# Kernel tuning notes

Hardware: AMD Instinct MI355X
Metric: run time of the kernel (lower is better)

Reference implementation:

```python
import jax, jax.numpy as jnp
import numpy as np

DIM = 4096
N_HEAD = 32
N_KV_HEAD = 8
HEAD_DIM = DIM // N_HEAD  # 128
B, T = 2, 2048


def _rope_freqs(T, head_dim, theta=10000.0):
    inv = 1.0 / (theta ** (np.arange(0, head_dim, 2, dtype=np.float32) / head_dim))
    t = np.arange(T, dtype=np.float32)
    ang = np.outer(t, inv)  # [T, head_dim/2]
    return jnp.asarray(np.stack([np.cos(ang), np.sin(ang)], axis=-1))  # [T, hd/2, 2]


def setup_inputs() -> dict:
    key = jax.random.key(0)
    ks = jax.random.split(key, 5)
    s = 1.0 / np.sqrt(DIM)
    return {
        "x": jax.random.normal(ks[0], (B, T, DIM), dtype=jnp.float32),
        "freqs_cis": _rope_freqs(T, HEAD_DIM),
        "wq": jax.random.normal(ks[1], (DIM, N_HEAD * HEAD_DIM), dtype=jnp.float32) * s,
        "wk": jax.random.normal(ks[2], (DIM, N_KV_HEAD * HEAD_DIM), dtype=jnp.float32) * s,
        "wv": jax.random.normal(ks[3], (DIM, N_KV_HEAD * HEAD_DIM), dtype=jnp.float32) * s,
        "wo": jax.random.normal(ks[4], (DIM, DIM), dtype=jnp.float32) * s,
    }


def _apply_rotary(x, freqs_cis):
    # x: [B, T, H, head_dim]; freqs_cis: [T, head_dim/2, 2]
    xs = x.reshape(*x.shape[:-1], -1, 2)  # [B, T, H, hd/2, 2]
    fc = freqs_cis[None, :, None, :, :]   # [1, T, 1, hd/2, 2]
    real = xs[..., 0] * fc[..., 0] - xs[..., 1] * fc[..., 1]
    imag = xs[..., 1] * fc[..., 0] + xs[..., 0] * fc[..., 1]
    return jnp.stack([real, imag], axis=-1).reshape(x.shape)


def reference(x, freqs_cis, wq, wk, wv, wo):
    Bx, Tx, C = x.shape
    q = (x @ wq).reshape(Bx, Tx, N_HEAD, HEAD_DIM)
    k = (x @ wk).reshape(Bx, Tx, N_KV_HEAD, HEAD_DIM)
    v = (x @ wv).reshape(Bx, Tx, N_KV_HEAD, HEAD_DIM)
    q = _apply_rotary(q, freqs_cis)
    k = _apply_rotary(k, freqs_cis)
    # [B, H, T, hd]
    q = q.transpose(0, 2, 1, 3)
    k = k.transpose(0, 2, 1, 3)
    v = v.transpose(0, 2, 1, 3)
    # GQA: expand kv heads to match query heads
    rep = N_HEAD // N_KV_HEAD
    k = jnp.repeat(k, rep, axis=1)
    v = jnp.repeat(v, rep, axis=1)
    scale = 1.0 / np.sqrt(HEAD_DIM)
    scores = jnp.einsum("bhqd,bhkd->bhqk", q, k) * scale
    causal = jnp.tril(jnp.ones((Tx, Tx), dtype=bool))
    scores = jnp.where(causal[None, None], scores, jnp.float32(-1e30))
    attn = jax.nn.softmax(scores, axis=-1)
    y = jnp.einsum("bhqk,bhkd->bhqd", attn, v)
    y = y.transpose(0, 2, 1, 3).reshape(Bx, Tx, C)
    return y @ wo
```

## Files before the change

kernel.cpp:

```cpp
#include <hip/hip_runtime.h>

#define DIM  4096
#define NH   32
#define NKV  8
#define HD   128
#define BSZ  2
#define TSEQ 2048

typedef __bf16 bf16x8 __attribute__((ext_vector_type(8)));
typedef unsigned short ushort8v __attribute__((ext_vector_type(8)));
typedef float f32x4 __attribute__((ext_vector_type(4)));

typedef void GV __attribute__((address_space(1)));
typedef void LV __attribute__((address_space(3)));

__device__ __forceinline__ unsigned short f2bf(float f) {
  unsigned u = __builtin_bit_cast(unsigned, f);
  u += 0x7FFFu + ((u >> 16) & 1u);
  return (unsigned short)(u >> 16);
}
__device__ __forceinline__ float bf2f(unsigned short b) {
  unsigned u = ((unsigned)b) << 16;
  return __builtin_bit_cast(float, u);
}
__device__ __forceinline__ void gload16(const unsigned short* g, unsigned short* l) {
  __builtin_amdgcn_global_load_lds((GV*)g, (LV*)l, 16, 0, 0);
}
__device__ __forceinline__ f32x4 mfma16(bf16x8 a, bf16x8 b, f32x4 c) {
  return __builtin_amdgcn_mfma_f32_16x16x32_bf16(a, b, c, 0, 0, 0);
}
__device__ __forceinline__ bf16x8 lds8(const unsigned short* p) {
  return __builtin_bit_cast(bf16x8, *(const ushort8v*)p);
}

__global__ void detect_dtype(const unsigned int* __restrict__ fc, int* __restrict__ flag) {
  if (threadIdx.x == 0 && blockIdx.x == 0)
    *flag = (fc[0] == 0x3F800000u) ? 0 : 1;
}

__global__ void cast_x(const void* __restrict__ src, unsigned short* __restrict__ dst,
                       const int* __restrict__ flag) {
  long t = (long)blockIdx.x * 256 + threadIdx.x;
  if (*flag) {
    ((uint2*)dst)[t] = ((const uint2*)src)[t];
  } else {
    float4 f = ((const float4*)src)[t];
    ushort4 o;
    o.x = f2bf(f.x); o.y = f2bf(f.y); o.z = f2bf(f.z); o.w = f2bf(f.w);
    ((ushort4*)dst)[t] = o;
  }
}

__global__ __launch_bounds__(256) void transpose64(const void* __restrict__ src,
                                                   unsigned short* __restrict__ dst,
                                                   int R, int C, const int* __restrict__ flag) {
  __shared__ unsigned short tile[64][68];
  const int isbf = *flag;
  const int tid = threadIdx.x;
  const int c0g = blockIdx.x * 64, r0g = blockIdx.y * 64;
  const int cc = (tid & 15) * 4;
  if (isbf) {
    const unsigned short* s = (const unsigned short*)src;
#pragma unroll
    for (int it = 0; it < 4; ++it) {
      const int r = it * 16 + (tid >> 4);
      ushort4 v = *(const ushort4*)(s + (long)(r0g + r) * C + c0g + cc);
      *(ushort4*)&tile[r][cc] = v;
    }
  } else {
    const float* s = (const float*)src;
#pragma unroll
    for (int it = 0; it < 4; ++it) {
      const int r = it * 16 + (tid >> 4);
      float4 f = *(const float4*)(s + (long)(r0g + r) * C + c0g + cc);
      ushort4 v;
      v.x = f2bf(f.x); v.y = f2bf(f.y); v.z = f2bf(f.z); v.w = f2bf(f.w);
      *(ushort4*)&tile[r][cc] = v;
    }
  }
  __syncthreads();
#pragma unroll
  for (int it = 0; it < 2; ++it) {
    const int c = (tid >> 3) + it * 32;
    const int r0 = (tid & 7) * 8;
    ushort8v o;
#pragma unroll
    for (int u = 0; u < 8; ++u) o[u] = tile[r0 + u][c];
    *(ushort8v*)(dst + (long)(c0g + c) * R + r0g + r0) = o;
  }
}

__device__ __forceinline__ void gemm128_loop(const unsigned short* __restrict__ A,
                                             const unsigned short* __restrict__ Bt,
                                             unsigned short* As, unsigned short* Bs,
                                             long tileM, long tileN, f32x4 (&acc)[4][4]) {
  const int tid = (int)threadIdx.x;
  const int lane = tid & 63, wave = tid >> 6;
  const int wr = wave >> 1, wc = wave & 1;
  const int lm = lane & 15, quad = lane >> 4;
  const int sr = tid >> 3;
  const int schunk = ((tid & 7) ^ (sr & 7)) * 8;
  const unsigned short* Ag = A + (tileM + sr) * 4096L + schunk;
  const unsigned short* Bg = Bt + (tileN + sr) * 4096L + schunk;
  unsigned short* Al = As + sr * 64 + (tid & 7) * 8;
  unsigned short* Bl = Bs + sr * 64 + (tid & 7) * 8;

  auto stgA = [&](int slot, int half, int tt) {
    const unsigned short* g = Ag + (long)half * (64 * 4096L) + (long)tt * 64;
    unsigned short* l = Al + slot * 8192 + half * 4096;
    gload16(g, l);
    gload16(g + 32 * 4096L, l + 2048);
  };
  auto stgB = [&](int slot, int half, int tt) {
    const unsigned short* g = Bg + (long)half * (64 * 4096L) + (long)tt * 64;
    unsigned short* l = Bl + slot * 8192 + half * 4096;
    gload16(g, l);
    gload16(g + 32 * 4096L, l + 2048);
  };
  auto rdA = [&](int so, int f, int kk) {
    return lds8(&As[so + (wr * 64 + f * 16 + lm) * 64 + (((kk * 4 + quad) ^ (lm & 7)) * 8)]);
  };
  auto rdB = [&](int so, int f, int kk) {
    return lds8(&Bs[so + (wc * 64 + f * 16 + lm) * 64 + (((kk * 4 + quad) ^ (lm & 7)) * 8)]);
  };

  stgB(0, 0, 0); stgB(0, 1, 0); stgA(0, 0, 0); stgA(0, 1, 0);
  stgB(1, 0, 1); stgB(1, 1, 1); stgA(1, 0, 1);
  asm volatile("s_waitcnt vmcnt(6)" ::: "memory");
  __builtin_amdgcn_sched_barrier(0);
  __builtin_amdgcn_s_barrier();

#pragma unroll 2
  for (int t = 0; t < 64; ++t) {
    __builtin_amdgcn_sched_barrier(0);
    const int s = t & 1;
    const int so = s * 8192;
    bf16x8 a[4][2], b[4][2];
#pragma unroll
    for (int f = 0; f < 4; ++f) { a[f][0] = rdA(so, f, 0); a[f][1] = rdA(so, f, 1); }
#pragma unroll
    for (int f = 0; f < 4; ++f) { b[f][0] = rdB(so, f, 0); b[f][1] = rdB(so, f, 1); }
    if (t < 63) stgA(s ^ 1, 1, t + 1);
    asm volatile("s_waitcnt lgkmcnt(0)" ::: "memory");
    __builtin_amdgcn_sched_barrier(0);
    __builtin_amdgcn_s_setprio(1);
#pragma unroll
    for (int mf = 0; mf < 4; ++mf)
#pragma unroll
      for (int nf = 0; nf < 4; ++nf)
        acc[mf][nf] = mfma16(a[mf][0], b[nf][0], acc[mf][nf]);
    __builtin_amdgcn_s_setprio(0);
    __builtin_amdgcn_sched_barrier(0);
    __builtin_amdgcn_s_barrier();
    if (t < 62) { stgB(s, 0, t + 2); stgB(s, 1, t + 2); stgA(s, 0, t + 2); }
    __builtin_amdgcn_s_setprio(1);
#pragma unroll
    for (int mf = 0; mf < 4; ++mf)
#pragma unroll
      for (int nf = 0; nf < 4; ++nf)
        acc[mf][nf] = mfma16(a[mf][1], b[nf][1], acc[mf][nf]);
    __builtin_amdgcn_s_setprio(0);
    if (t < 62)       asm volatile("s_waitcnt vmcnt(6)" ::: "memory");
    else if (t == 62) asm volatile("s_waitcnt vmcnt(0)" ::: "memory");
    __builtin_amdgcn_sched_barrier(0);
    __builtin_amdgcn_s_barrier();
  }
}

__global__ __launch_bounds__(256, 2) void gemm_qkv8(const unsigned short* __restrict__ A,
                                                    const unsigned short* __restrict__ Bt,
                                                    const void* __restrict__ fcv,
                                                    const int* __restrict__ flag,
                                                    unsigned short* __restrict__ qo,
                                                    unsigned short* __restrict__ ko,
                                                    unsigned short* __restrict__ vo) {
  __shared__ __align__(16) unsigned short As[2 * 8192];
  __shared__ __align__(16) unsigned short Bs[2 * 8192];
  const int bid = (int)blockIdx.x;
  const int xcd = bid & 7, idx = bid >> 3;
  const int band = idx >> 6;
  const int rr = idx & 63;
  const long tileM = (long)((xcd & 3) * 8 + (rr & 7)) * 128;
  const long tileN = (long)((xcd >> 2) * 24 + band * 8 + (rr >> 3)) * 128;
  f32x4 acc[4][4] = {};
  gemm128_loop(A, Bt, As, Bs, tileM, tileN, acc);
  const int tid = (int)threadIdx.x;
  const int lane = tid & 63, wave = tid >> 6;
  const int wr = wave >> 1, wc = wave & 1;
  const int lm = lane & 15, quad = lane >> 4;
  const int isbf = *flag;
  const int nb = (int)tileN + wc * 64;
  if (nb < 5120) {
    const int isk = (nb >= 4096);
    unsigned short* dst = isk ? ko : qo;
    const int hpb = isk ? NKV : NH;
    const int coff = isk ? 4096 : 0;
#pragma unroll
    for (int mf = 0; mf < 4; ++mf)
#pragma unroll
      for (int r = 0; r < 4; ++r) {
        const int m = (int)tileM + wr * 64 + mf * 16 + quad * 4 + r;
        const int b = m >> 11, tq = m & (TSEQ - 1);
#pragma unroll
        for (int nf = 0; nf < 4; ++nf) {
          const int n = nb + nf * 16 + lm;
          float val = acc[mf][nf][r];
          float par = __shfl_xor(val, 1);
          const int ip = (n & 127) >> 1;
          const long fo = (long)tq * 64 + ip;
          float cz, sz;
          if (isbf) {
            const unsigned short* fu = (const unsigned short*)fcv;
            cz = bf2f(fu[fo * 2]); sz = bf2f(fu[fo * 2 + 1]);
          } else {
            float2 cs = ((const float2*)fcv)[fo];
            cz = cs.x; sz = cs.y;
          }
          float out = (n & 1) ? (val * cz + par * sz) : (val * cz - par * sz);
          const int h = (n - coff) >> 7, d = n & 127;
          dst[((long)(b * hpb + h) * TSEQ + tq) * HD + d] = f2bf(out);
        }
      }
  } else {
#pragma unroll
    for (int mf = 0; mf < 4; ++mf)
#pragma unroll
      for (int r = 0; r < 4; ++r) {
        const int m = (int)tileM + wr * 64 + mf * 16 + quad * 4 + r;
        const int b = m >> 11, tq = m & (TSEQ - 1);
#pragma unroll
        for (int nf = 0; nf < 4; ++nf) {
          const int n = nb + nf * 16 + lm;
          const int h = (n - 5120) >> 7, d = n & 127;
          vo[((long)(b * NKV + h) * HD + d) * TSEQ + tq] = f2bf(acc[mf][nf][r]);
        }
      }
  }
}

__global__ __launch_bounds__(256, 2) void gemm_wo8(const unsigned short* __restrict__ A,
                                                   const unsigned short* __restrict__ Bt,
                                                   void* __restrict__ Cv,
                                                   const int* __restrict__ flag) {
  __shared__ __align__(16) unsigned short As[2 * 8192];
  __shared__ __align__(16) unsigned short Bs[2 * 8192];
  const int bid = (int)blockIdx.x;
  const int xcd = bid & 7, idx = bid >> 3;
  const int band = idx >> 6;
  const int rr = idx & 63;
  const long tileM = (long)((xcd & 3) * 8 + (rr & 7)) * 128;
  const long tileN = (long)((xcd >> 2) * 16 + band * 8 + (rr >> 3)) * 128;
  f32x4 acc[4][4] = {};
  gemm128_loop(A, Bt, As, Bs, tileM, tileN, acc);
  const int tid = (int)threadIdx.x;
  const int lane = tid & 63, wave = tid >> 6;
  const int wr = wave >> 1, wc = wave & 1;
  const int lm = lane & 15, quad = lane >> 4;
  const int obf = *flag;
  const long N = 4096;
  if (obf) {
    unsigned short* C = (unsigned short*)Cv;
#pragma unroll
    for (int mf = 0; mf < 4; ++mf)
#pragma unroll
      for (int nf = 0; nf < 4; ++nf)
#pragma unroll
        for (int r = 0; r < 4; ++r)
          C[(tileM + wr * 64 + mf * 16 + quad * 4 + r) * N + tileN + wc * 64 + nf * 16 + lm] =
              f2bf(acc[mf][nf][r]);
  } else {
    float* C = (float*)Cv;
#pragma unroll
    for (int mf = 0; mf < 4; ++mf)
#pragma unroll
      for (int nf = 0; nf < 4; ++nf)
#pragma unroll
        for (int r = 0; r < 4; ++r)
          C[(tileM + wr * 64 + mf * 16 + quad * 4 + r) * N + tileN + wc * 64 + nf * 16 + lm] =
              acc[mf][nf][r];
  }
}

__global__ __launch_bounds__(512, 2) void flash_attn(const unsigned short* __restrict__ q,
                                                     const unsigned short* __restrict__ k,
                                                     const unsigned short* __restrict__ vT,
                                                     unsigned short* __restrict__ y) {
  __shared__ unsigned short Ks[2][32 * 128];
  __shared__ unsigned short Vs[2][128 * 32];
  __shared__ unsigned short Pl[8][32 * 40];
  const int tid = threadIdx.x;
  const int lane = tid & 63, wave = tid >> 6;
  const int lm = lane & 15, quad = lane >> 4;
  const int bid = (int)blockIdx.x;
  const int halfg = bid >> 8, jj = bid & 255;
  const int qt = jj >> 6, bh = jj & 63;
  const int qi = halfg ? qt : 7 - qt;
  const int b = bh >> 5, h = bh & 31, kvh = h >> 2;
  const int q0 = qi * 256;
  const unsigned short* Kb = k + (long)(b * NKV + kvh) * TSEQ * HD;
  const unsigned short* Vb = vT + (long)(b * NKV + kvh) * HD * TSEQ;
  const unsigned short* Qb = q + ((long)(b * NH + h) * TSEQ + q0 + wave * 32) * HD;
  bf16x8 qf[2][4];
#pragma unroll
  for (int mi = 0; mi < 2; ++mi)
#pragma unroll
    for (int ks = 0; ks < 4; ++ks)
      qf[mi][ks] = __builtin_bit_cast(bf16x8,
          *(const ushort8v*)(Qb + (mi * 16 + lm) * HD + ks * 32 + quad * 8));
  f32x4 o[2][8] = {};
  float li[2][4] = {};
  const float scale = 0.08838834764831845f;
  const int krow = tid >> 4, kcl = ((tid & 15) ^ (krow & 7)) * 8;
  const int vrow = tid >> 2, vcl = ((tid & 3) ^ ((vrow >> 1) & 3)) * 8;
  const int ktiles = qi * 8 + 8;
  {
    gload16(Kb + krow * HD + kcl, &Ks[0][tid * 8]);
    gload16(Vb + (long)vrow * TSEQ + vcl, &Vs[0][tid * 8]);
  }
  for (int kt = 0; kt < ktiles; ++kt) {
    __syncthreads();
    if (kt + 1 < ktiles) {
      const int bi = (kt + 1) & 1;
      const unsigned short* Kg = Kb + (long)(kt + 1) * 32 * HD;
      gload16(Kg + krow * HD + kcl, &Ks[bi][tid * 8]);
      const unsigned short* Vg = Vb + (kt + 1) * 32;
      gload16(Vg + (long)vrow * TSEQ + vcl, &Vs[bi][tid * 8]);
    }
    const unsigned short* KsB = Ks[kt & 1];
    const unsigned short* VsB = Vs[kt & 1];
    f32x4 s[2][2] = {};
#pragma unroll
    for (int ni = 0; ni < 2; ++ni)
#pragma unroll
      for (int ks = 0; ks < 4; ++ks) {
        bf16x8 kf = lds8(&KsB[(ni * 16 + lm) * 128 + ((ks * 4 + quad) ^ (lm & 7)) * 8]);
        s[0][ni] = mfma16(qf[0][ks], kf, s[0][ni]);
        s[1][ni] = mfma16(qf[1][ks], kf, s[1][ni]);
      }
    unsigned short* PlW = &Pl[wave][0];
#pragma unroll
    for (int mi = 0; mi < 2; ++mi)
#pragma unroll
      for (int r = 0; r < 4; ++r) {
        const int qg = q0 + wave * 32 + mi * 16 + quad * 4 + r;
#pragma unroll
        for (int ni = 0; ni < 2; ++ni) {
          const int kg = kt * 32 + ni * 16 + lm;
          float p = (kg <= qg) ? __expf(s[mi][ni][r] * scale) : 0.f;
          li[mi][r] += p;
          PlW[(mi * 16 + quad * 4 + r) * 40 + ni * 16 + lm] = f2bf(p);
        }
      }
    bf16x8 pf0 = lds8(&PlW[lm * 40 + quad * 8]);
    bf16x8 pf1 = lds8(&PlW[(16 + lm) * 40 + quad * 8]);
#pragma unroll
    for (int db = 0; db < 8; ++db) {
      bf16x8 vf = lds8(&VsB[(db * 16 + lm) * 32 + (quad ^ ((lm >> 1) & 3)) * 8]);
      o[0][db] = mfma16(pf0, vf, o[0][db]);
      o[1][db] = mfma16(pf1, vf, o[1][db]);
    }
  }
  float inv[2][4];
#pragma unroll
  for (int mi = 0; mi < 2; ++mi)
#pragma unroll
    for (int r = 0; r < 4; ++r) {
      float l = li[mi][r];
      l += __shfl_xor(l, 1, 16);
      l += __shfl_xor(l, 2, 16);
      l += __shfl_xor(l, 4, 16);
      l += __shfl_xor(l, 8, 16);
      inv[mi][r] = 1.0f / l;
    }
  unsigned short* yo = y + ((long)b * TSEQ + q0 + wave * 32) * DIM + h * 128 + lm;
#pragma unroll
  for (int mi = 0; mi < 2; ++mi)
#pragma unroll
    for (int r = 0; r < 4; ++r) {
      unsigned short* yr = yo + (long)(mi * 16 + quad * 4 + r) * DIM;
#pragma unroll
      for (int db = 0; db < 8; ++db)
        yr[db * 16] = f2bf(o[mi][db][r] * inv[mi][r]);
    }
}

extern "C" void kernel_launch(void* const* d_in, const int* in_sizes, int n_in,
                              void* d_out, int out_size, void* d_ws, size_t ws_size,
                              hipStream_t stream) {
  const void* x  = d_in[0];
  const void* fc = d_in[1];
  const void* wq = d_in[2];
  const void* wk = d_in[3];
  const void* wv = d_in[4];
  const void* wo = d_in[5];
  char* ws = (char*)d_ws;
  int* flag             = (int*)ws;
  unsigned short* xb    = (unsigned short*)(ws + 256);
  unsigned short* wqkvT = xb + 16777216L;
  unsigned short* woT   = wqkvT + 25165824L;
  unsigned short* qb    = woT + 16777216L;
  unsigned short* kb    = qb + 16777216L;
  unsigned short* vb    = kb + 4194304L;
  unsigned short* yb    = xb;

  detect_dtype<<<dim3(1), dim3(64), 0, stream>>>((const unsigned int*)fc, flag);
  cast_x<<<dim3(16384), dim3(256), 0, stream>>>(x, xb, flag);
  transpose64<<<dim3(64, 64), dim3(256), 0, stream>>>(wq, wqkvT, 4096, 4096, flag);
  transpose64<<<dim3(16, 64), dim3(256), 0, stream>>>(wk, wqkvT + 4096L * 4096, 4096, 1024, flag);
  transpose64<<<dim3(16, 64), dim3(256), 0, stream>>>(wv, wqkvT + 5120L * 4096, 4096, 1024, flag);
  transpose64<<<dim3(64, 64), dim3(256), 0, stream>>>(wo, woT, 4096, 4096, flag);
  gemm_qkv8<<<dim3(1536), dim3(256), 0, stream>>>(xb, wqkvT, fc, flag, qb, kb, vb);
  flash_attn<<<dim3(512), dim3(512), 0, stream>>>(qb, kb, vb, yb);
  gemm_wo8<<<dim3(1024), dim3(256), 0, stream>>>(yb, woT, d_out, flag);
}
```

Before: 734.2 us.

## Stream K/V directly from global in attention, fold softmax scale into Q

Attention blocks shrink to 256 threads with 128-row query tiles and 1024 blocks. The shared-memory double-buffered K/V staging and its barriers are removed, and each wave reads K and V straight from global memory (lds8 used on global pointers). Each wave runs only up to its own causal diagonal tile, and the mask is applied only on that last tile. The 1/sqrt(d) scale is folded into Q in the QKV GEMM epilogue. This drops syncs and LDS traffic but loses cross-wave reuse of K/V tiles, relying on cache hits for the repeated global loads.

```diff
diff --git a/kernel.cpp b/kernel.cpp
--- a/kernel.cpp
+++ b/kernel.cpp
@@ -195,6 +195,7 @@
     unsigned short* dst = isk ? ko : qo;
     const int hpb = isk ? NKV : NH;
     const int coff = isk ? 4096 : 0;
+    const float qs = isk ? 1.0f : 0.08838834764831845f;
 #pragma unroll
     for (int mf = 0; mf < 4; ++mf)
 #pragma unroll
@@ -218,7 +219,7 @@
           }
           float out = (n & 1) ? (val * cz + par * sz) : (val * cz - par * sz);
           const int h = (n - coff) >> 7, d = n & 127;
-          dst[((long)(b * hpb + h) * TSEQ + tq) * HD + d] = f2bf(out);
+          dst[((long)(b * hpb + h) * TSEQ + tq) * HD + d] = f2bf(out * qs);
         }
       }
   } else {
@@ -281,22 +282,19 @@
   }
 }
 
-__global__ __launch_bounds__(512, 2) void flash_attn(const unsigned short* __restrict__ q,
+__global__ __launch_bounds__(256, 3) void flash_attn(const unsigned short* __restrict__ q,
                                                      const unsigned short* __restrict__ k,
                                                      const unsigned short* __restrict__ vT,
                                                      unsigned short* __restrict__ y) {
-  __shared__ unsigned short Ks[2][32 * 128];
-  __shared__ unsigned short Vs[2][128 * 32];
-  __shared__ unsigned short Pl[8][32 * 40];
+  __shared__ unsigned short Pl[4][32 * 40];
   const int tid = threadIdx.x;
   const int lane = tid & 63, wave = tid >> 6;
   const int lm = lane & 15, quad = lane >> 4;
   const int bid = (int)blockIdx.x;
-  const int halfg = bid >> 8, jj = bid & 255;
-  const int qt = jj >> 6, bh = jj & 63;
-  const int qi = halfg ? qt : 7 - qt;
+  const int qt = bid >> 6, bh = bid & 63;
+  const int qi = 15 - qt;
   const int b = bh >> 5, h = bh & 31, kvh = h >> 2;
-  const int q0 = qi * 256;
+  const int q0 = qi * 128;
   const unsigned short* Kb = k + (long)(b * NKV + kvh) * TSEQ * HD;
   const unsigned short* Vb = vT + (long)(b * NKV + kvh) * HD * TSEQ;
   const unsigned short* Qb = q + ((long)(b * NH + h) * TSEQ + q0 + wave * 32) * HD;
@@ -309,53 +307,52 @@
           *(const ushort8v*)(Qb + (mi * 16 + lm) * HD + ks * 32 + quad * 8));
   f32x4 o[2][8] = {};
   float li[2][4] = {};
-  const float scale = 0.08838834764831845f;
-  const int krow = tid >> 4, kcl = ((tid & 15) ^ (krow & 7)) * 8;
-  const int vrow = tid >> 2, vcl = ((tid & 3) ^ ((vrow >> 1) & 3)) * 8;
-  const int ktiles = qi * 8 + 8;
-  {
-    gload16(Kb + krow * HD + kcl, &Ks[0][tid * 8]);
-    gload16(Vb + (long)vrow * TSEQ + vcl, &Vs[0][tid * 8]);
-  }
-  for (int kt = 0; kt < ktiles; ++kt) {
-    __syncthreads();
-    if (kt + 1 < ktiles) {
-      const int bi = (kt + 1) & 1;
-      const unsigned short* Kg = Kb + (long)(kt + 1) * 32 * HD;
-      gload16(Kg + krow * HD + kcl, &Ks[bi][tid * 8]);
-      const unsigned short* Vg = Vb + (kt + 1) * 32;
-      gload16(Vg + (long)vrow * TSEQ + vcl, &Vs[bi][tid * 8]);
-    }
-    const unsigned short* KsB = Ks[kt & 1];
-    const unsigned short* VsB = Vs[kt & 1];
+  const int mylast = qi * 4 + wave;
+  unsigned short* PlW = &Pl[wave][0];
+
+  for (int kt = 0; kt <= mylast; ++kt) {
+    const unsigned short* Kt = Kb + (long)kt * 32 * HD;
     f32x4 s[2][2] = {};
 #pragma unroll
     for (int ni = 0; ni < 2; ++ni)
 #pragma unroll
       for (int ks = 0; ks < 4; ++ks) {
-        bf16x8 kf = lds8(&KsB[(ni * 16 + lm) * 128 + ((ks * 4 + quad) ^ (lm & 7)) * 8]);
+        bf16x8 kf = lds8(Kt + (ni * 16 + lm) * HD + ks * 32 + quad * 8);
         s[0][ni] = mfma16(qf[0][ks], kf, s[0][ni]);
         s[1][ni] = mfma16(qf[1][ks], kf, s[1][ni]);
       }
-    unsigned short* PlW = &Pl[wave][0];
-#pragma unroll
-    for (int mi = 0; mi < 2; ++mi)
-#pragma unroll
-      for (int r = 0; r < 4; ++r) {
-        const int qg = q0 + wave * 32 + mi * 16 + quad * 4 + r;
-#pragma unroll
-        for (int ni = 0; ni < 2; ++ni) {
-          const int kg = kt * 32 + ni * 16 + lm;
-          float p = (kg <= qg) ? __expf(s[mi][ni][r] * scale) : 0.f;
-          li[mi][r] += p;
-          PlW[(mi * 16 + quad * 4 + r) * 40 + ni * 16 + lm] = f2bf(p);
+    if (kt < mylast) {
+#pragma unroll
+      for (int mi = 0; mi < 2; ++mi)
+#pragma unroll
+        for (int r = 0; r < 4; ++r)
+#pragma unroll
+          for (int ni = 0; ni < 2; ++ni) {
+            float p = __expf(s[mi][ni][r]);
+            li[mi][r] += p;
+            PlW[(mi * 16 + quad * 4 + r) * 40 + ni * 16 + lm] = f2bf(p);
+          }
+    } else {
+#pragma unroll
+      for (int mi = 0; mi < 2; ++mi)
+#pragma unroll
+        for (int r = 0; r < 4; ++r) {
+          const int rowo = mi * 16 + quad * 4 + r;
+#pragma unroll
+          for (int ni = 0; ni < 2; ++ni) {
+            const int colo = ni * 16 + lm;
+            float p = (colo <= rowo) ? __expf(s[mi][ni][r]) : 0.f;
+            li[mi][r] += p;
+            PlW[rowo * 40 + colo] = f2bf(p);
+          }
         }
-      }
+    }
     bf16x8 pf0 = lds8(&PlW[lm * 40 + quad * 8]);
     bf16x8 pf1 = lds8(&PlW[(16 + lm) * 40 + quad * 8]);
+    const unsigned short* Vt = Vb + kt * 32;
 #pragma unroll
     for (int db = 0; db < 8; ++db) {
-      bf16x8 vf = lds8(&VsB[(db * 16 + lm) * 32 + (quad ^ ((lm >> 1) & 3)) * 8]);
+      bf16x8 vf = lds8(Vt + (long)(db * 16 + lm) * TSEQ + quad * 8);
       o[0][db] = mfma16(pf0, vf, o[0][db]);
       o[1][db] = mfma16(pf1, vf, o[1][db]);
     }
@@ -410,6 +407,6 @@
   transpose64<<<dim3(16, 64), dim3(256), 0, stream>>>(wv, wqkvT + 5120L * 4096, 4096, 1024, flag);
   transpose64<<<dim3(64, 64), dim3(256), 0, stream>>>(wo, woT, 4096, 4096, flag);
   gemm_qkv8<<<dim3(1536), dim3(256), 0, stream>>>(xb, wqkvT, fc, flag, qb, kb, vb);
-  flash_attn<<<dim3(512), dim3(512), 0, stream>>>(qb, kb, vb, yb);
+  flash_attn<<<dim3(1024), dim3(256), 0, stream>>>(qb, kb, vb, yb);
   gemm_wo8<<<dim3(1024), dim3(256), 0, stream>>>(yb, woT, d_out, flag);
 }
```

Result: slower. 853.7 us (+16.3%).
